# Optimization experiments

Measured on AMD Instinct MI355X. Metric: run time of the kernel, lower is better.

Reference implementation:

```python
import jax, jax.numpy as jnp
import numpy as np

# Bernstein-basis theta coefficients for d=2 (calculate_theta2(2)),
# inv_coeff order: [x^0, x^1, x^2]
THETAS = ((3.0, -3.0, 0.75), (0.0, 3.0, -1.5), (0.0, 0.0, 0.75))
HIGH_ORDER = 2

N_NODES = 50000
N_EDGES = 800000
IN_DIM, HID_DIM, OUT_DIM = 128, 64, 2


def setup_inputs() -> dict:
    key = jax.random.key(0)
    ks = jax.random.split(key, 16)
    f32 = jnp.float32
    def w(k, shape, fan_in):
        return jax.random.normal(k, shape, dtype=f32) * (1.0 / np.sqrt(fan_in))
    return {
        "in_feat": jax.random.normal(ks[0], (N_NODES, IN_DIM), dtype=f32),
        "src": jax.random.randint(ks[1], (N_EDGES,), 0, N_NODES, dtype=jnp.int32),
        "dst": jax.random.randint(ks[2], (N_EDGES,), 0, N_NODES, dtype=jnp.int32),
        "W1": w(ks[3], (IN_DIM, HID_DIM), IN_DIM), "b1": jnp.zeros((HID_DIM,), f32),
        "W2": w(ks[4], (HID_DIM, HID_DIM), HID_DIM), "b2": jnp.zeros((HID_DIM,), f32),
        "W3": w(ks[5], (HID_DIM * 5, HID_DIM), HID_DIM * 5), "b3": jnp.zeros((HID_DIM,), f32),
        "W4": w(ks[6], (HID_DIM, OUT_DIM), HID_DIM), "b4": jnp.zeros((OUT_DIM,), f32),
        "Wg1": w(ks[7], (IN_DIM, HID_DIM), IN_DIM), "bg1": jnp.zeros((HID_DIM,), f32),
        "Wg2": w(ks[8], (HID_DIM, IN_DIM), HID_DIM), "bg2": jnp.zeros((IN_DIM,), f32),
    }


def _spmm(x, src, dst, n):
    # y[v] = sum_{(u,v) in E} x[u]   (DGL update_all(copy_u, sum))
    return jax.ops.segment_sum(x[src], dst, num_segments=n)


def reference(in_feat, src, dst, W1, b1, W2, b2, W3, b3, W4, b4, Wg1, bg1, Wg2, bg2):
    n = in_feat.shape[0]
    ones_e = jnp.ones(src.shape[0], dtype=in_feat.dtype)
    deg_in = jnp.clip(jax.ops.segment_sum(ones_e, dst, num_segments=n), 1.0)
    deg_out = jnp.clip(jax.ops.segment_sum(ones_e, src, num_segments=n), 1.0)
    din = (deg_in ** -0.5)[:, None]   # [N,1]
    dout = (deg_out ** -0.5)[:, None]

    def lap(f):
        # f - D^{-1/2} A D^{-1/2} f  (in-degree norm, as in unnLaplacian)
        return f - _spmm(f * din, src, dst, n) * din

    # MLP front-end
    h = jax.nn.relu(in_feat @ W1 + b1)
    h = jax.nn.relu(h @ W2 + b2)

    branches = []
    # BandConv branches (lin=False): theta-weighted Laplacian polynomial
    for theta in THETAS:
        f = h
        acc = theta[0] * h
        for k in range(1, len(theta)):
            f = lap(f)
            acc = acc + theta[k] * f
        branches.append(acc)
    # HighConv branches: repeated Laplacian, num_layer = 1..HIGH_ORDER
    f = h
    for j in range(HIGH_ORDER):
        f = lap(f)
        branches.append(f)

    h_final = jnp.concatenate(branches, axis=-1)  # [N, 5*hid]
    out = jax.nn.relu(h_final @ W3 + b3) @ W4 + b4  # [N, out_dim]

    # GCN branch on self-loop-free graph (same edges here): symmetric norm GraphConv
    def gconv(x, W, b):
        return _spmm(x * dout, src, dst, n) * din @ W + b
    emb = gconv(jax.nn.relu(gconv(in_feat, Wg1, bg1)), Wg2, bg2)  # [N, in_dim]

    return out, emb
```

## Files before the change

### kernel.cpp

```cpp
#include <hip/hip_runtime.h>
#include <hip/hip_bf16.h>
#include <math.h>

#define NN 50000
#define NE 800000
#define C128 128
#define CE 6250
#define NR 8
#define RNOD 6250
#define RW 3125
#define NW 25000
#define HISTB 1024
#define INITB 160
#define RB 98
#define GB 782
#define ZSB 782
#define FSG 3125

typedef _Float16 half8 __attribute__((ext_vector_type(8)));
typedef float f32x4 __attribute__((ext_vector_type(4)));
typedef unsigned short ushort4v __attribute__((ext_vector_type(4)));

static inline int cdiv(int a, int b) { return (a + b - 1) / b; }


__device__ inline size_t pack_pos(int k, int n, int K, int M) {
    int tile = n >> 4;
    int kstep = k >> 5;
    int quad = (k >> 3) & 3;
    int j = k & 7;
    int lane = (quad << 4) | (n & 15);
    return ((size_t)(tile * (K >> 5) + kstep) * 64 + lane) * 8 + j;
}

__device__ void pack_std_dev(int bx, const float* __restrict__ W, _Float16* __restrict__ Wpk,
                             int K, int M) {
    int idx = bx * 256 + threadIdx.x;
    if (idx >= K * M) return;
    int k = idx / M, n = idx % M;
    Wpk[pack_pos(k, n, K, M)] = (_Float16)W[idx];
}

__device__ void pack_wc_dev(int bx, const float* __restrict__ W3, _Float16* __restrict__ wcpk) {
    int idx = bx * 256 + threadIdx.x;
    if (idx >= 3 * 4096) return;
    int b = idx >> 12;
    int rem = idx & 4095;
    int k = rem >> 6, n = rem & 63;
    float w0 = W3[(0 * 64 + k) * 64 + n];
    float w1 = W3[(1 * 64 + k) * 64 + n];
    float w2 = W3[(2 * 64 + k) * 64 + n];
    float w3 = W3[(3 * 64 + k) * 64 + n];
    float w4 = W3[(4 * 64 + k) * 64 + n];
    float v;
    if (b == 0)      v = 3.f * w0;
    else if (b == 1) v = -3.f * w0 + 3.f * w1 + w3;
    else             v = 0.75f * w0 - 1.5f * w1 + 0.75f * w2 + w4;
    wcpk[pack_pos(b * 64 + k, n, 192, 64)] = (_Float16)v;
}

__device__ void init_dev(int bx,
                         const float* __restrict__ W1, _Float16* __restrict__ W1pk,
                         const float* __restrict__ W2, _Float16* __restrict__ W2pk,
                         const float* __restrict__ Wg1, _Float16* __restrict__ Wg1pk,
                         const float* __restrict__ Wg2, _Float16* __restrict__ Wg2pk,
                         const float* __restrict__ W3, _Float16* __restrict__ wcpk) {
    if (bx < 32) { pack_std_dev(bx, W1, W1pk, 128, 64); return; }
    bx -= 32;
    if (bx < 16) { pack_std_dev(bx, W2, W2pk, 64, 64); return; }
    bx -= 16;
    if (bx < 32) { pack_std_dev(bx, Wg1, Wg1pk, 128, 64); return; }
    bx -= 32;
    if (bx < 32) { pack_std_dev(bx, Wg2, Wg2pk, 64, 128); return; }
    bx -= 32;
    pack_wc_dev(bx, W3, wcpk);
}


__device__ void hist_dev(int bx, const int* __restrict__ idx, unsigned* __restrict__ H,
                         unsigned* __restrict__ cnt) {
    int c = bx & 127, r = bx >> 7;
    int tid = threadIdx.x;
    for (int j = tid; j < RW; j += 256) cnt[j] = 0;
    __syncthreads();
    int lo = r * RNOD;
    const int* p = idx + (size_t)c * CE;
    for (int i = tid; i < CE; i += 256) {
        int v = p[i] - lo;
        if ((unsigned)v < (unsigned)RNOD)
            atomicAdd(&cnt[v >> 1], 1u << ((v & 1) * 16));
    }
    __syncthreads();
    unsigned* outp = H + (size_t)c * NW + r * RW;
    for (int j = tid; j < RW; j += 256) outp[j] = cnt[j];
}

__device__ void reduce_dev(int bx, const unsigned* __restrict__ H, int* __restrict__ dgo,
                           float* __restrict__ o_rsq, float* __restrict__ o_inv,
                           float* __restrict__ o_sq) {
    int w = bx * 256 + threadIdx.x;
    if (w >= NW) return;
    unsigned slo = 0, shi = 0;
#pragma unroll 8
    for (int c = 0; c < C128; c++) {
        unsigned h = H[(size_t)c * NW + w];
        slo += h & 0xffffu; shi += h >> 16;
    }
    if (dgo) {
        dgo[2 * w]     = slo > 64u ? 64 : (int)slo;
        dgo[2 * w + 1] = shi > 64u ? 64 : (int)shi;
    }
    float f0 = (float)(slo < 1u ? 1u : slo);
    float f1 = (float)(shi < 1u ? 1u : shi);
    o_rsq[2 * w] = rsqrtf(f0); o_rsq[2 * w + 1] = rsqrtf(f1);
    if (o_inv) { o_inv[2 * w] = 1.f / f0; o_inv[2 * w + 1] = 1.f / f1; }
    if (o_sq)  { o_sq[2 * w] = sqrtf(f0); o_sq[2 * w + 1] = sqrtf(f1); }
}

__device__ void prefix_dev(int bx, const unsigned* __restrict__ HD, unsigned* __restrict__ baseD) {
    int w = bx * 256 + threadIdx.x;
    if (w >= NW) return;
    unsigned slo = 0, shi = 0;
#pragma unroll 8
    for (int c = 0; c < C128; c++) {
        unsigned b0 = slo > 64u ? 64u : slo;
        unsigned b1 = shi > 64u ? 64u : shi;
        baseD[(size_t)c * NW + w] = b0 | (b1 << 16);
        unsigned h = HD[(size_t)c * NW + w];
        slo += h & 0xffffu; shi += h >> 16;
    }
}

__device__ void scatter_dev(int bx, const int* __restrict__ src, const int* __restrict__ dst,
                            const unsigned* __restrict__ baseD,
                            unsigned short* __restrict__ colsPad,
                            unsigned* __restrict__ cnt) {
    int c = bx & 127, r = bx >> 7;
    int tid = threadIdx.x;
    const unsigned* bslice = baseD + (size_t)c * NW + r * RW;
    for (int j = tid; j < RW; j += 256) cnt[j] = bslice[j];
    __syncthreads();
    int lo = r * RNOD;
    const int* pd = dst + (size_t)c * CE;
    const int* ps = src + (size_t)c * CE;
    for (int i = tid; i < CE; i += 256) {
        int v = pd[i];
        int lv = v - lo;
        if ((unsigned)lv < (unsigned)RNOD) {
            int sh = (lv & 1) * 16;
            unsigned old = atomicAdd(&cnt[lv >> 1], 1u << sh);
            unsigned pos = (old >> sh) & 0xffffu;
            if (pos < 64u) colsPad[(size_t)v * 64 + pos] = (unsigned short)ps[i];
        }
    }
}

__device__ void zscale_dev(int bx, half8* __restrict__ pair, const float* __restrict__ dout, int N) {
    int idx = bx * 256 + threadIdx.x;
    if (idx >= N * 4) return;
    int row = idx >> 2, q = idx & 3;
    float m = dout[row];
    half8* z = pair + (size_t)row * 16 + 8 + q * 2;
    half8 a = z[0], b = z[1];
#pragma unroll
    for (int j = 0; j < 8; j++) {
        a[j] = (_Float16)((float)a[j] * m);
        b[j] = (_Float16)((float)b[j] * m);
    }
    z[0] = a; z[1] = b;
}


struct HSegs { const _Float16* p[3]; int ld[3]; };

template <int M, int K, bool OUTW, bool RSCA>
__device__ void mg_dev(int bx, HSegs A, const half8* __restrict__ Wpk,
                       const float* __restrict__ bias, int relu,
                       float* __restrict__ C,
                       _Float16* __restrict__ Ch0, const float* __restrict__ ms0,
                       const float* __restrict__ rsc,
                       const float* __restrict__ W4, const float* __restrict__ b4,
                       float* __restrict__ outp, int ldC, int N) {
    constexpr int NT = M / 16;
    constexpr int NKS = K / 32;
    int tid = threadIdx.x;
    int wave = tid >> 6, lane = tid & 63;
    int quad = lane >> 4, m = lane & 15;
    int row0 = bx * 64 + wave * 16;
    int rowA = row0 + m; if (rowA >= N) rowA = N - 1;
    _Float16 hs = (_Float16)1.f;
    if (RSCA) hs = (_Float16)rsc[rowA];
    f32x4 acc[NT];
#pragma unroll
    for (int t = 0; t < NT; t++) acc[t] = (f32x4){0.f, 0.f, 0.f, 0.f};
#pragma unroll
    for (int ks = 0; ks < NKS; ks++) {
        const _Float16* ap = A.p[ks >> 1] + (size_t)rowA * A.ld[ks >> 1] + (ks & 1) * 32 + quad * 8;
        half8 af = *(const half8*)ap;
        if (RSCA) {
#pragma unroll
            for (int j = 0; j < 8; j++) af[j] *= hs;
        }
#pragma unroll
        for (int t = 0; t < NT; t++) {
            half8 bf = Wpk[(t * NKS + ks) * 64 + lane];
            acc[t] = __builtin_amdgcn_mfma_f32_16x16x32_f16(af, bf, acc[t], 0, 0, 0);
        }
    }
    float outv[NT][4];
#pragma unroll
    for (int t = 0; t < NT; t++) {
        float bv = bias ? bias[t * 16 + m] : 0.f;
#pragma unroll
        for (int r = 0; r < 4; r++) {
            float v = acc[t][r] + bv;
            if (relu) v = fmaxf(v, 0.f);
            outv[t][r] = v;
        }
    }
    if (OUTW) {
        float w40[NT], w41[NT];
#pragma unroll
        for (int t = 0; t < NT; t++) {
            w40[t] = W4[(t * 16 + m) * 2];
            w41[t] = W4[(t * 16 + m) * 2 + 1];
        }
#pragma unroll
        for (int r = 0; r < 4; r++) {
            float p0 = 0.f, p1 = 0.f;
#pragma unroll
            for (int t = 0; t < NT; t++) {
                p0 += outv[t][r] * w40[t];
                p1 += outv[t][r] * w41[t];
            }
#pragma unroll
            for (int off = 1; off < 16; off <<= 1) {
                p0 += __shfl_xor(p0, off);
                p1 += __shfl_xor(p1, off);
            }
            int row = row0 + quad * 4 + r;
            if (m == 0 && row < N) {
                outp[(size_t)row * 2 + 0] = p0 + b4[0];
                outp[(size_t)row * 2 + 1] = p1 + b4[1];
            }
        }
    }
    if (C || Ch0) {
#pragma unroll
        for (int r = 0; r < 4; r++) {
            int row = row0 + quad * 4 + r;
            if (row >= N) continue;
            float m0 = (Ch0 && ms0) ? ms0[row] : 1.f;
#pragma unroll
            for (int t = 0; t < NT; t++) {
                size_t off = (size_t)row * ldC + t * 16 + m;
                if (C)   C[off] = outv[t][r];
                if (Ch0) Ch0[off] = (_Float16)(outv[t][r] * m0);
            }
        }
    }
}

__device__ void a15_dev(int bx, const float* __restrict__ in_feat,
                        const half8* __restrict__ W1pk, const half8* __restrict__ Wg1pk,
                        const float* __restrict__ b1,
                        _Float16* __restrict__ h1h, _Float16* __restrict__ zh, int N) {
    int tid = threadIdx.x;
    int wave = tid >> 6, lane = tid & 63;
    int quad = lane >> 4, m = lane & 15;
    int row0 = bx * 64 + wave * 16;
    int rowA = row0 + m; if (rowA >= N) rowA = N - 1;
    f32x4 acc0[4], acc1[4];
#pragma unroll
    for (int t = 0; t < 4; t++) {
        acc0[t] = (f32x4){0.f, 0.f, 0.f, 0.f};
        acc1[t] = (f32x4){0.f, 0.f, 0.f, 0.f};
    }
#pragma unroll
    for (int ks = 0; ks < 4; ks++) {
        const float* ap = in_feat + (size_t)rowA * 128 + ks * 32 + quad * 8;
        float4 u = *(const float4*)ap;
        float4 v = *(const float4*)(ap + 4);
        half8 af;
        af[0] = (_Float16)u.x; af[1] = (_Float16)u.y; af[2] = (_Float16)u.z; af[3] = (_Float16)u.w;
        af[4] = (_Float16)v.x; af[5] = (_Float16)v.y; af[6] = (_Float16)v.z; af[7] = (_Float16)v.w;
#pragma unroll
        for (int t = 0; t < 4; t++) {
            acc0[t] = __builtin_amdgcn_mfma_f32_16x16x32_f16(af, W1pk[(t * 4 + ks) * 64 + lane], acc0[t], 0, 0, 0);
            acc1[t] = __builtin_amdgcn_mfma_f32_16x16x32_f16(af, Wg1pk[(t * 4 + ks) * 64 + lane], acc1[t], 0, 0, 0);
        }
    }
#pragma unroll
    for (int r = 0; r < 4; r++) {
        int row = row0 + quad * 4 + r;
        if (row >= N) continue;
#pragma unroll
        for (int t = 0; t < 4; t++) {
            float v0 = fmaxf(acc0[t][r] + b1[t * 16 + m], 0.f);
            h1h[(size_t)row * 64 + t * 16 + m] = (_Float16)v0;
            zh[(size_t)row * 128 + t * 16 + m] = (_Float16)acc1[t][r];
        }
    }
}


__launch_bounds__(256)
__global__ void k_L1(const float* __restrict__ W1, _Float16* __restrict__ W1pk,
                     const float* __restrict__ W2, _Float16* __restrict__ W2pk,
                     const float* __restrict__ Wg1, _Float16* __restrict__ Wg1pk,
                     const float* __restrict__ Wg2, _Float16* __restrict__ Wg2pk,
                     const float* __restrict__ W3, _Float16* __restrict__ wcpk,
                     const int* __restrict__ src, const int* __restrict__ dst,
                     unsigned* __restrict__ HD, unsigned* __restrict__ HS) {
    __shared__ unsigned cnt[RW];
    int bx = blockIdx.x;
    if (bx < INITB) { init_dev(bx, W1, W1pk, W2, W2pk, Wg1, Wg1pk, Wg2, Wg2pk, W3, wcpk); return; }
    bx -= INITB;
    if (bx < HISTB) { hist_dev(bx, dst, HD, cnt); return; }
    bx -= HISTB;
    hist_dev(bx, src, HS, cnt);
}

__launch_bounds__(256)
__global__ void k_L2(const unsigned* __restrict__ HD, const unsigned* __restrict__ HS,
                     int* __restrict__ degin, float* __restrict__ din,
                     float* __restrict__ din2, float* __restrict__ dsq,
                     float* __restrict__ dout, unsigned* __restrict__ baseD,
                     const float* __restrict__ in_feat,
                     const half8* __restrict__ W1pk, const half8* __restrict__ Wg1pk,
                     const float* __restrict__ b1,
                     _Float16* __restrict__ h1h, _Float16* __restrict__ zh, int N) {
    int bx = blockIdx.x;
    if (bx < RB) { reduce_dev(bx, HD, degin, din, din2, dsq); return; }
    bx -= RB;
    if (bx < RB) { reduce_dev(bx, HS, nullptr, dout, nullptr, nullptr); return; }
    bx -= RB;
    if (bx < RB) { prefix_dev(bx, HD, baseD); return; }
    bx -= RB;
    a15_dev(bx, in_feat, W1pk, Wg1pk, b1, h1h, zh, N);
}

__launch_bounds__(256)
__global__ void k_L3(const int* __restrict__ src, const int* __restrict__ dst,
                     const unsigned* __restrict__ baseD, unsigned short* __restrict__ colsPad,
                     const _Float16* __restrict__ h1h, const half8* __restrict__ W2pk,
                     const float* __restrict__ b2, _Float16* __restrict__ pair0h,
                     const float* __restrict__ din,
                     half8* __restrict__ pair0v, const float* __restrict__ dout, int N) {
    __shared__ unsigned cnt[RW];
    int bx = blockIdx.x;
    if (bx < HISTB) { scatter_dev(bx, src, dst, baseD, colsPad, cnt); return; }
    bx -= HISTB;
    if (bx < GB) {
        HSegs A;
        A.p[0] = h1h; A.ld[0] = 64;
        A.p[1] = nullptr; A.ld[1] = 0;
        A.p[2] = nullptr; A.ld[2] = 0;
        mg_dev<64, 64, false, false>(bx, A, W2pk, b2, 1, nullptr, pair0h, din,
                                     nullptr, nullptr, nullptr, nullptr, 128, N);
        return;
    }
    bx -= GB;
    zscale_dev(bx, pair0v, dout, N);
}


struct FSP {
    const half8* xp;
    half8* uOut; int uld;
    half8* zOut; int zld;
    const float* din2;
    const float* zrs1;
    const float* bgz;
    const float* zrs2;
    int zrelu;
};

__launch_bounds__(256)
__global__ void k_FS(FSP P, const unsigned short* __restrict__ colsPad,
                     const int* __restrict__ deg, int N) {
    int g = blockIdx.x;
    int tid = threadIdx.x;
    int wave = tid >> 6, lane = tid & 63;
    int grp = lane >> 4, c = lane & 15;
    int row = g * 16 + wave * 4 + grp;
    if (row >= N) return;
    int dg = deg[row];
    const unsigned short* cp = colsPad + (size_t)row * 64;
    float acc[8];
#pragma unroll
    for (int j = 0; j < 8; j++) acc[j] = 0.f;
    int e = 0;
    for (; e + 7 < dg; e += 8) {
        ushort4v sa = *(const ushort4v*)(cp + e);
        ushort4v sb = *(const ushort4v*)(cp + e + 4);
        half8 v0 = P.xp[(size_t)sa.x * 16 + c];
        half8 v1 = P.xp[(size_t)sa.y * 16 + c];
        half8 v2 = P.xp[(size_t)sa.z * 16 + c];
        half8 v3 = P.xp[(size_t)sa.w * 16 + c];
        half8 v4 = P.xp[(size_t)sb.x * 16 + c];
        half8 v5 = P.xp[(size_t)sb.y * 16 + c];
        half8 v6 = P.xp[(size_t)sb.z * 16 + c];
        half8 v7 = P.xp[(size_t)sb.w * 16 + c];
#pragma unroll
        for (int j = 0; j < 8; j++) {
            acc[j] += (float)v0[j] + (float)v1[j] + (float)v2[j] + (float)v3[j]
                    + (float)v4[j] + (float)v5[j] + (float)v6[j] + (float)v7[j];
        }
    }
    for (; e + 3 < dg; e += 4) {
        ushort4v ss = *(const ushort4v*)(cp + e);
        half8 v0 = P.xp[(size_t)ss.x * 16 + c];
        half8 v1 = P.xp[(size_t)ss.y * 16 + c];
        half8 v2 = P.xp[(size_t)ss.z * 16 + c];
        half8 v3 = P.xp[(size_t)ss.w * 16 + c];
#pragma unroll
        for (int j = 0; j < 8; j++)
            acc[j] += (float)v0[j] + (float)v1[j] + (float)v2[j] + (float)v3[j];
    }
    for (; e < dg; e++) {
        int s = cp[e];
        half8 v = P.xp[(size_t)s * 16 + c];
#pragma unroll
        for (int j = 0; j < 8; j++) acc[j] += (float)v[j];
    }
    half8 h;
    if (c < 8) {
        float d = P.din2[row];
        half8 f = P.xp[(size_t)row * 16 + c];
#pragma unroll
        for (int j = 0; j < 8; j++)
            h[j] = (_Float16)((float)f[j] - acc[j] * d);
        P.uOut[(size_t)row * P.uld + c] = h;
    } else {
        float s1 = P.zrs1[row];
#pragma unroll
        for (int j = 0; j < 8; j++) acc[j] *= s1;
        if (P.bgz) {
            const float* bb = P.bgz + (c - 8) * 8;
#pragma unroll
            for (int j = 0; j < 8; j++) acc[j] += bb[j];
        }
        if (P.zrelu) {
#pragma unroll
            for (int j = 0; j < 8; j++) acc[j] = fmaxf(acc[j], 0.f);
        }
        float s2 = P.zrs2 ? P.zrs2[row] : 1.f;
#pragma unroll
        for (int j = 0; j < 8; j++) h[j] = (_Float16)(acc[j] * s2);
        P.zOut[(size_t)row * P.zld + (c - 8)] = h;
    }
}

__launch_bounds__(256)
__global__ void k_F3(const _Float16* __restrict__ pair0, const _Float16* __restrict__ pair1,
                     const _Float16* __restrict__ u2h, const half8* __restrict__ wcpk,
                     const float* __restrict__ b3, const float* __restrict__ dsq,
                     const float* __restrict__ W4, const float* __restrict__ b4,
                     float* __restrict__ outp,
                     const _Float16* __restrict__ sgh, const half8* __restrict__ Wg2pk,
                     const float* __restrict__ bg2, float* __restrict__ emb, int N) {
    int bx = blockIdx.x;
    if (bx < GB) {
        HSegs A;
        A.p[0] = pair0; A.ld[0] = 128;
        A.p[1] = pair1; A.ld[1] = 128;
        A.p[2] = u2h;   A.ld[2] = 64;
        mg_dev<64, 192, true, true>(bx, A, wcpk, b3, 1, nullptr, nullptr, nullptr,
                                    dsq, W4, b4, outp, 64, N);
        return;
    }
    bx -= GB;
    HSegs A;
    A.p[0] = sgh; A.ld[0] = 64;
    A.p[1] = nullptr; A.ld[1] = 0;
    A.p[2] = nullptr; A.ld[2] = 0;
    mg_dev<128, 64, false, false>(bx, A, Wg2pk, bg2, 0, emb, nullptr, nullptr,
                                  nullptr, nullptr, nullptr, nullptr, 128, N);
}

extern "C" void kernel_launch(void* const* d_in, const int* in_sizes, int n_in,
                              void* d_out, int out_size, void* d_ws, size_t ws_size,
                              hipStream_t stream) {
    const int N = NN;
    const float* in_feat = (const float*)d_in[0];
    const int* src = (const int*)d_in[1];
    const int* dst = (const int*)d_in[2];
    const float* W1 = (const float*)d_in[3];
    const float* b1 = (const float*)d_in[4];
    const float* W2 = (const float*)d_in[5];
    const float* b2 = (const float*)d_in[6];
    const float* W3 = (const float*)d_in[7];
    const float* b3 = (const float*)d_in[8];
    const float* W4 = (const float*)d_in[9];
    const float* b4 = (const float*)d_in[10];
    const float* Wg1 = (const float*)d_in[11];
    const float* bg1 = (const float*)d_in[12];
    const float* Wg2 = (const float*)d_in[13];
    const float* bg2 = (const float*)d_in[14];

    float* out = (float*)d_out;
    float* emb = out + (size_t)N * 2;

    float* fw = (float*)d_ws;
    float* din  = fw;
    float* din2 = din + N;
    float* dsq  = din2 + N;
    float* dout = dsq + N;
    int* degin  = (int*)(dout + N);
    unsigned short* colsPad = (unsigned short*)(degin + N);
    unsigned* HD   = (unsigned*)(colsPad + (size_t)64 * N);
    unsigned* HS   = HD + (size_t)C128 * NW;
    unsigned* baseD = HS + (size_t)C128 * NW;
    _Float16* hp = (_Float16*)(baseD + (size_t)C128 * NW);
    _Float16* h1h   = hp;
    _Float16* pair0 = h1h + (size_t)64 * N;
    _Float16* pair1 = pair0 + (size_t)128 * N;
    _Float16* u2h   = pair1 + (size_t)128 * N;
    _Float16* sgh   = u2h + (size_t)64 * N;
    _Float16* W1pk  = sgh + (size_t)64 * N;
    _Float16* W2pk  = W1pk + 8192;
    _Float16* Wg1pk = W2pk + 4096;
    _Float16* Wg2pk = Wg1pk + 8192;
    _Float16* wcpk  = Wg2pk + 8192;

    k_L1<<<INITB + 2 * HISTB, 256, 0, stream>>>(W1, W1pk, W2, W2pk, Wg1, Wg1pk,
        Wg2, Wg2pk, W3, wcpk, src, dst, HD, HS);

    k_L2<<<3 * RB + GB, 256, 0, stream>>>(HD, HS, degin, din, din2, dsq, dout, baseD,
        in_feat, (const half8*)W1pk, (const half8*)Wg1pk, b1, h1h, pair0 + 64, N);

    k_L3<<<HISTB + GB + ZSB, 256, 0, stream>>>(src, dst, baseD, colsPad,
        h1h, (const half8*)W2pk, b2, pair0, din, (half8*)pair0, dout, N);

    FSP p;
    p = {(const half8*)pair0, (half8*)pair1, 16, (half8*)pair1 + 8, 16,
         din2, din, bg1, dout, 1};
    k_FS<<<FSG, 256, 0, stream>>>(p, colsPad, degin, N);

    p = {(const half8*)pair1, (half8*)u2h, 8, (half8*)sgh, 8,
         din2, din, nullptr, nullptr, 0};
    k_FS<<<FSG, 256, 0, stream>>>(p, colsPad, degin, N);

    k_F3<<<2 * GB, 256, 0, stream>>>(pair0, pair1, u2h, (const half8*)wcpk, b3, dsq,
        W4, b4, out, sgh, (const half8*)Wg2pk, bg2, emb, N);
}
```

Baseline: 252.6 us.

## Move first-layer GEMMs into launch 1 with per-block LDS weight packing

The first MLP and GCN input GEMMs (W1, Wg1) now run in the first kernel launch, alongside the degree histograms. Each block converts and packs the fp32 weights into shared memory itself, which drops the global pre-packing step. This lets the dense GEMM overlap with the histogram work and shrinks the second launch to just the reductions and prefix sums. In exchange, each GEMM block redundantly converts 16K weight elements and adds syncthreads; the shared buffer is resized to 16 KB and reused by the histogram path.

```diff
diff --git a/kernel.cpp b/kernel.cpp
--- a/kernel.cpp
+++ b/kernel.cpp
@@ -11,7 +11,7 @@
 #define RW 3125
 #define NW 25000
 #define HISTB 1024
-#define INITB 160
+#define INITB 96
 #define RB 98
 #define GB 782
 #define ZSB 782
@@ -60,17 +60,11 @@
 }
 
 __device__ void init_dev(int bx,
-                         const float* __restrict__ W1, _Float16* __restrict__ W1pk,
                          const float* __restrict__ W2, _Float16* __restrict__ W2pk,
-                         const float* __restrict__ Wg1, _Float16* __restrict__ Wg1pk,
                          const float* __restrict__ Wg2, _Float16* __restrict__ Wg2pk,
                          const float* __restrict__ W3, _Float16* __restrict__ wcpk) {
-    if (bx < 32) { pack_std_dev(bx, W1, W1pk, 128, 64); return; }
-    bx -= 32;
     if (bx < 16) { pack_std_dev(bx, W2, W2pk, 64, 64); return; }
     bx -= 16;
-    if (bx < 32) { pack_std_dev(bx, Wg1, Wg1pk, 128, 64); return; }
-    bx -= 32;
     if (bx < 32) { pack_std_dev(bx, Wg2, Wg2pk, 64, 128); return; }
     bx -= 32;
     pack_wc_dev(bx, W3, wcpk);
@@ -262,82 +256,100 @@
 }
 
 __device__ void a15_dev(int bx, const float* __restrict__ in_feat,
-                        const half8* __restrict__ W1pk, const half8* __restrict__ Wg1pk,
+                        const float* __restrict__ W1, const float* __restrict__ Wg1,
                         const float* __restrict__ b1,
-                        _Float16* __restrict__ h1h, _Float16* __restrict__ zh, int N) {
+                        _Float16* __restrict__ h1h, _Float16* __restrict__ zh,
+                        _Float16* __restrict__ wsm, int N) {
     int tid = threadIdx.x;
     int wave = tid >> 6, lane = tid & 63;
     int quad = lane >> 4, m = lane & 15;
     int row0 = bx * 64 + wave * 16;
     int rowA = row0 + m; if (rowA >= N) rowA = N - 1;
-    f32x4 acc0[4], acc1[4];
-#pragma unroll
-    for (int t = 0; t < 4; t++) {
-        acc0[t] = (f32x4){0.f, 0.f, 0.f, 0.f};
-        acc1[t] = (f32x4){0.f, 0.f, 0.f, 0.f};
-    }
+    half8 af[4];
 #pragma unroll
     for (int ks = 0; ks < 4; ks++) {
         const float* ap = in_feat + (size_t)rowA * 128 + ks * 32 + quad * 8;
         float4 u = *(const float4*)ap;
         float4 v = *(const float4*)(ap + 4);
-        half8 af;
-        af[0] = (_Float16)u.x; af[1] = (_Float16)u.y; af[2] = (_Float16)u.z; af[3] = (_Float16)u.w;
-        af[4] = (_Float16)v.x; af[5] = (_Float16)v.y; af[6] = (_Float16)v.z; af[7] = (_Float16)v.w;
-#pragma unroll
-        for (int t = 0; t < 4; t++) {
-            acc0[t] = __builtin_amdgcn_mfma_f32_16x16x32_f16(af, W1pk[(t * 4 + ks) * 64 + lane], acc0[t], 0, 0, 0);
-            acc1[t] = __builtin_amdgcn_mfma_f32_16x16x32_f16(af, Wg1pk[(t * 4 + ks) * 64 + lane], acc1[t], 0, 0, 0);
-        }
-    }
+        af[ks][0] = (_Float16)u.x; af[ks][1] = (_Float16)u.y;
+        af[ks][2] = (_Float16)u.z; af[ks][3] = (_Float16)u.w;
+        af[ks][4] = (_Float16)v.x; af[ks][5] = (_Float16)v.y;
+        af[ks][6] = (_Float16)v.z; af[ks][7] = (_Float16)v.w;
+    }
+    const half8* wf = (const half8*)wsm;
+    f32x4 acc[4];
+    for (int i = tid; i < 8192; i += 256)
+        wsm[pack_pos(i >> 6, i & 63, 128, 64)] = (_Float16)W1[i];
+    __syncthreads();
+#pragma unroll
+    for (int t = 0; t < 4; t++) acc[t] = (f32x4){0.f, 0.f, 0.f, 0.f};
+#pragma unroll
+    for (int ks = 0; ks < 4; ks++)
+#pragma unroll
+        for (int t = 0; t < 4; t++)
+            acc[t] = __builtin_amdgcn_mfma_f32_16x16x32_f16(af[ks], wf[(t * 4 + ks) * 64 + lane], acc[t], 0, 0, 0);
 #pragma unroll
     for (int r = 0; r < 4; r++) {
         int row = row0 + quad * 4 + r;
         if (row >= N) continue;
 #pragma unroll
-        for (int t = 0; t < 4; t++) {
-            float v0 = fmaxf(acc0[t][r] + b1[t * 16 + m], 0.f);
-            h1h[(size_t)row * 64 + t * 16 + m] = (_Float16)v0;
-            zh[(size_t)row * 128 + t * 16 + m] = (_Float16)acc1[t][r];
-        }
+        for (int t = 0; t < 4; t++)
+            h1h[(size_t)row * 64 + t * 16 + m] = (_Float16)fmaxf(acc[t][r] + b1[t * 16 + m], 0.f);
+    }
+    __syncthreads();
+    for (int i = tid; i < 8192; i += 256)
+        wsm[pack_pos(i >> 6, i & 63, 128, 64)] = (_Float16)Wg1[i];
+    __syncthreads();
+#pragma unroll
+    for (int t = 0; t < 4; t++) acc[t] = (f32x4){0.f, 0.f, 0.f, 0.f};
+#pragma unroll
+    for (int ks = 0; ks < 4; ks++)
+#pragma unroll
+        for (int t = 0; t < 4; t++)
+            acc[t] = __builtin_amdgcn_mfma_f32_16x16x32_f16(af[ks], wf[(t * 4 + ks) * 64 + lane], acc[t], 0, 0, 0);
+#pragma unroll
+    for (int r = 0; r < 4; r++) {
+        int row = row0 + quad * 4 + r;
+        if (row >= N) continue;
+#pragma unroll
+        for (int t = 0; t < 4; t++)
+            zh[(size_t)row * 128 + t * 16 + m] = (_Float16)acc[t][r];
     }
 }
 
 
 __launch_bounds__(256)
-__global__ void k_L1(const float* __restrict__ W1, _Float16* __restrict__ W1pk,
+__global__ void k_L1(const float* __restrict__ in_feat,
+                     const float* __restrict__ W1, const float* __restrict__ Wg1,
+                     const float* __restrict__ b1,
+                     _Float16* __restrict__ h1h, _Float16* __restrict__ zh,
                      const float* __restrict__ W2, _Float16* __restrict__ W2pk,
-                     const float* __restrict__ Wg1, _Float16* __restrict__ Wg1pk,
                      const float* __restrict__ Wg2, _Float16* __restrict__ Wg2pk,
                      const float* __restrict__ W3, _Float16* __restrict__ wcpk,
                      const int* __restrict__ src, const int* __restrict__ dst,
-                     unsigned* __restrict__ HD, unsigned* __restrict__ HS) {
-    __shared__ unsigned cnt[RW];
+                     unsigned* __restrict__ HD, unsigned* __restrict__ HS, int N) {
+    __shared__ _Float16 smh[8192];
     int bx = blockIdx.x;
-    if (bx < INITB) { init_dev(bx, W1, W1pk, W2, W2pk, Wg1, Wg1pk, Wg2, Wg2pk, W3, wcpk); return; }
+    if (bx < GB) { a15_dev(bx, in_feat, W1, Wg1, b1, h1h, zh, smh, N); return; }
+    bx -= GB;
+    if (bx < INITB) { init_dev(bx, W2, W2pk, Wg2, Wg2pk, W3, wcpk); return; }
     bx -= INITB;
-    if (bx < HISTB) { hist_dev(bx, dst, HD, cnt); return; }
+    if (bx < HISTB) { hist_dev(bx, dst, HD, (unsigned*)smh); return; }
     bx -= HISTB;
-    hist_dev(bx, src, HS, cnt);
+    hist_dev(bx, src, HS, (unsigned*)smh);
 }
 
 __launch_bounds__(256)
 __global__ void k_L2(const unsigned* __restrict__ HD, const unsigned* __restrict__ HS,
                      int* __restrict__ degin, float* __restrict__ din,
                      float* __restrict__ din2, float* __restrict__ dsq,
-                     float* __restrict__ dout, unsigned* __restrict__ baseD,
-                     const float* __restrict__ in_feat,
-                     const half8* __restrict__ W1pk, const half8* __restrict__ Wg1pk,
-                     const float* __restrict__ b1,
-                     _Float16* __restrict__ h1h, _Float16* __restrict__ zh, int N) {
+                     float* __restrict__ dout, unsigned* __restrict__ baseD) {
     int bx = blockIdx.x;
     if (bx < RB) { reduce_dev(bx, HD, degin, din, din2, dsq); return; }
     bx -= RB;
     if (bx < RB) { reduce_dev(bx, HS, nullptr, dout, nullptr, nullptr); return; }
     bx -= RB;
-    if (bx < RB) { prefix_dev(bx, HD, baseD); return; }
-    bx -= RB;
-    a15_dev(bx, in_feat, W1pk, Wg1pk, b1, h1h, zh, N);
+    prefix_dev(bx, HD, baseD);
 }
 
 __launch_bounds__(256)
@@ -518,17 +530,14 @@
     _Float16* pair1 = pair0 + (size_t)128 * N;
     _Float16* u2h   = pair1 + (size_t)128 * N;
     _Float16* sgh   = u2h + (size_t)64 * N;
-    _Float16* W1pk  = sgh + (size_t)64 * N;
-    _Float16* W2pk  = W1pk + 8192;
-    _Float16* Wg1pk = W2pk + 4096;
-    _Float16* Wg2pk = Wg1pk + 8192;
+    _Float16* W2pk  = sgh + (size_t)64 * N;
+    _Float16* Wg2pk = W2pk + 4096;
     _Float16* wcpk  = Wg2pk + 8192;
 
-    k_L1<<<INITB + 2 * HISTB, 256, 0, stream>>>(W1, W1pk, W2, W2pk, Wg1, Wg1pk,
-        Wg2, Wg2pk, W3, wcpk, src, dst, HD, HS);
-
-    k_L2<<<3 * RB + GB, 256, 0, stream>>>(HD, HS, degin, din, din2, dsq, dout, baseD,
-        in_feat, (const half8*)W1pk, (const half8*)Wg1pk, b1, h1h, pair0 + 64, N);
+    k_L1<<<GB + INITB + 2 * HISTB, 256, 0, stream>>>(in_feat, W1, Wg1, b1,
+        h1h, pair0 + 64, W2, W2pk, Wg2, Wg2pk, W3, wcpk, src, dst, HD, HS, N);
+
+    k_L2<<<3 * RB, 256, 0, stream>>>(HD, HS, degin, din, din2, dsq, dout, baseD);
 
     k_L3<<<HISTB + GB + ZSB, 256, 0, stream>>>(src, dst, baseD, colsPad,
         h1h, (const half8*)W2pk, b2, pair0, din, (half8*)pair0, dout, N);
```

After: 248.3 us. Within noise of the previous version (-1.7%).
